# Performance work log

Measured on AMD Instinct MI355X. Metric: run time of the kernel, lower is better.

Reference implementation:

```python
import jax, jax.numpy as jnp
import numpy as np

N_E = 1024      # nconcepts (codebook size)
E_DIM = 64      # cdim (codebook vector dim)
BETA = 0.25
LEGACY = True


def setup_inputs() -> dict:
    key = jax.random.key(0)
    k1, k2, k3 = jax.random.split(key, 3)
    z_ = jax.random.normal(k1, (32, 256, 32, 32), jnp.float32)
    # 1x1 conv dis_modulator: 256 -> 64 channels (stored as [out, in])
    conv_w = jax.random.normal(k2, (64, 256), jnp.float32) / np.sqrt(256.0)
    conv_b = jnp.zeros((64,), jnp.float32)
    # embedding.weight.data.uniform_(-1/n_e, 1/n_e)
    emb = jax.random.uniform(k3, (N_E, E_DIM), jnp.float32, -1.0 / N_E, 1.0 / N_E)
    return {"z_": z_, "conv_w": conv_w, "conv_b": conv_b, "emb": emb}


def _forward(z_, conv_w, conv_b, emb):
    sg = jax.lax.stop_gradient
    # dis_modulator: 1x1 conv == per-pixel linear map  (B,Cin,H,W)->(B,Cout,H,W)
    z = jnp.einsum('bchw,oc->bohw', z_, conv_w) + conv_b[None, :, None, None]
    B = z.shape[0]
    # torch .view(-1, e_dim): row-major flatten of (B,C,H,W) into chunks of e_dim
    zf = z.reshape(-1, E_DIM)  # [B*C*H*W/e_dim, e_dim]

    # contrastive term: mean pairwise cosine similarity of codebook rows
    d1 = emb @ emb.T                                  # [n_e, n_e]
    norms = jnp.linalg.norm(emb, axis=1)              # [n_e]
    cosine = d1 / (norms[:, None] * norms[None, :])
    contrastive = jnp.mean(cosine)

    # squared L2 distances: ||z||^2 + ||e||^2 - 2 z.e
    d = (jnp.sum(zf * zf, axis=1, keepdims=True)
         + jnp.sum(emb * emb, axis=1)[None, :]
         - 2.0 * (zf @ emb.T))                        # [N, n_e]
    idx = jnp.argmin(d, axis=1)                       # [N]
    z_q = emb[idx].reshape(z.shape)

    if LEGACY:
        loss = jnp.mean((sg(z_q) - z) ** 2) + BETA * jnp.mean((z_q - sg(z)) ** 2)
    else:
        loss = BETA * jnp.mean((sg(z_q) - z) ** 2) + jnp.mean((z_q - sg(z)) ** 2)
    # hessian_penalty(G, z_, G_z=z): G is an affine 1x1 conv, so the central
    # second difference G(z+x) - 2G(z) + G(z-x) is identically zero -> penalty = 0.
    loss = loss + contrastive

    # straight-through estimator
    z_q_st = z + sg(z_q - z)

    # replicate source exactly: flat zeros(B*n_e) scattered at codebook indices
    sampled = jnp.zeros((B * N_E,), z.dtype).at[idx].set(1.0).reshape(B, N_E)
    min_idx = idx.reshape(B, -1)
    return z_q_st, loss, sampled, min_idx


def reference(z_, conv_w, conv_b, emb):
    z_q, loss, sampled, min_idx = _forward(z_, conv_w, conv_b, emb)
    return z_q, loss, sampled, min_idx
```

## Files before the change

### kernel.cpp

```cpp
#include <hip/hip_runtime.h>

#define BATCH   32
#define CIN     256
#define COUT    64
#define HW      1024
#define NE      1024
#define ED      64
#define ZTOT    2097152

#define OFF_LOSS 2097152
#define OFF_SAMP 2097153
#define OFF_IDX  2129921

#define CXSTR 68
#define XSTR  68
#define ESTR  132

__global__ __launch_bounds__(256, 4) void k_pre(const float* __restrict__ x,
                                                const float* __restrict__ w,
                                                const float* __restrict__ bias,
                                                float* __restrict__ z,
                                                const float* __restrict__ emb,
                                                float* __restrict__ out_samp,
                                                float* __restrict__ enorm,
                                                float* __restrict__ cpart) {
    __shared__ float SH[64 * CXSTR * 2];
    int bx = blockIdx.x;
    int t  = threadIdx.x;

    if (bx < 512) {
        float* Xs = SH;
        float* Ws = SH + 64 * CXSTR;
        int b  = bx >> 4;
        int p0 = (bx & 15) * 64;
        int pg = t & 15;
        int og = t >> 4;
        float acc[4][4];
        #pragma unroll
        for (int i = 0; i < 4; i++)
            #pragma unroll
            for (int j = 0; j < 4; j++) acc[i][j] = 0.0f;

        for (int c0 = 0; c0 < CIN; c0 += 64) {
            __syncthreads();
            {
                int u = t & 15, cg2 = t >> 4;
                #pragma unroll
                for (int m = 0; m < 4; m++) {
                    int c = cg2 + 16 * m;
                    float4 v = *(const float4*)&x[(size_t)(b * CIN + c0 + c) * HW + p0 + 4 * u];
                    *(float4*)&Xs[c * CXSTR + 4 * u] = v;
                }
                #pragma unroll
                for (int m = 0; m < 4; m++) {
                    int o = cg2 + 16 * m;
                    float4 v = *(const float4*)&w[o * CIN + c0 + 4 * u];
                    Ws[(4 * u + 0) * CXSTR + o] = v.x;
                    Ws[(4 * u + 1) * CXSTR + o] = v.y;
                    Ws[(4 * u + 2) * CXSTR + o] = v.z;
                    Ws[(4 * u + 3) * CXSTR + o] = v.w;
                }
            }
            __syncthreads();
            #pragma unroll 8
            for (int k = 0; k < 64; k++) {
                float4 xv = *(const float4*)&Xs[k * CXSTR + 4 * pg];
                float4 wv = *(const float4*)&Ws[k * CXSTR + 4 * og];
                float xa[4] = {xv.x, xv.y, xv.z, xv.w};
                float wb[4] = {wv.x, wv.y, wv.z, wv.w};
                #pragma unroll
                for (int i = 0; i < 4; i++)
                    #pragma unroll
                    for (int j = 0; j < 4; j++)
                        acc[i][j] = fmaf(xa[i], wb[j], acc[i][j]);
            }
        }
        #pragma unroll
        for (int j = 0; j < 4; j++) {
            int o = 4 * og + j;
            float bv = bias[o];
            float4 out;
            out.x = acc[0][j] + bv;
            out.y = acc[1][j] + bv;
            out.z = acc[2][j] + bv;
            out.w = acc[3][j] + bv;
            *(float4*)&z[(size_t)(b * COUT + o) * HW + p0 + 4 * pg] = out;
        }
        return;
    }
    if (bx < 640) {
        out_samp[(bx - 512) * 256 + t] = 0.0f;
        return;
    }
    if (bx < 656) {
        float* invl = SH;
        float* S    = SH + 64;
        int b2 = bx - 640;
        int i0 = b2 * 64;
        if (t < 64) {
            const float* e = emb + (size_t)(i0 + t) * ED;
            float r8[8];
            #pragma unroll
            for (int s = 0; s < 8; s++) { float xx = e[s]; r8[s] = xx * xx; }
            #pragma unroll
            for (int m = 1; m < 8; m++) {
                #pragma unroll
                for (int s = 0; s < 8; s++) { float xx = e[8 * m + s]; r8[s] += xx * xx; }
            }
            float en = ((r8[0] + r8[1]) + (r8[2] + r8[3])) + ((r8[4] + r8[5]) + (r8[6] + r8[7]));
            invl[t] = 1.0f / sqrtf(en);
        }
        __syncthreads();
        int d = t & 63, q = t >> 6;
        float s = 0.0f;
        #pragma unroll
        for (int m = 0; m < 16; m++) {
            int il = q + 4 * m;
            s = fmaf(emb[(size_t)(i0 + il) * ED + d], invl[il], s);
        }
        S[t] = s;
        __syncthreads();
        if (t < 64)
            cpart[b2 * 64 + t] = (S[t] + S[t + 64]) + (S[t + 128] + S[t + 192]);
        return;
    }
    {
        int j = (bx - 656) * 256 + t;
        const float* e = emb + (size_t)j * ED;
        float r8[8];
        #pragma unroll
        for (int s = 0; s < 8; s++) { float xx = e[s]; r8[s] = xx * xx; }
        #pragma unroll
        for (int m = 1; m < 8; m++) {
            #pragma unroll
            for (int s = 0; s < 8; s++) { float xx = e[8 * m + s]; r8[s] += xx * xx; }
        }
        enorm[j] = ((r8[0] + r8[1]) + (r8[2] + r8[3])) + ((r8[4] + r8[5]) + (r8[6] + r8[7]));
    }
}

__global__ __launch_bounds__(256, 2) void k_dist(const float* __restrict__ z,
                                                 const float* __restrict__ emb,
                                                 const float* __restrict__ enorm,
                                                 float* __restrict__ out_idx,
                                                 float* __restrict__ out_samp,
                                                 float* __restrict__ out_zq,
                                                 float* __restrict__ ssep) {
    __shared__ float zs[64 * XSTR];
    __shared__ float es[64 * ESTR];
    __shared__ float zn_s[64];
    __shared__ float en_s[128];
    __shared__ float redd_s[16 * 64];
    __shared__ int   redj_s[16 * 64];
    __shared__ int   bj_s[64];
    __shared__ float warr[4];
    int t = threadIdx.x;
    int row0 = blockIdx.x * 64;
    int rg = t & 15;
    int cg = t >> 4;

    {
        int k = t & 63, wv = t >> 6;
        #pragma unroll
        for (int m = 0; m < 4; m++) {
            int v = wv + 4 * m;
            float4 val;
            val.x = z[(size_t)(row0 + 4 * v + 0) * ED + k];
            val.y = z[(size_t)(row0 + 4 * v + 1) * ED + k];
            val.z = z[(size_t)(row0 + 4 * v + 2) * ED + k];
            val.w = z[(size_t)(row0 + 4 * v + 3) * ED + k];
            *(float4*)&zs[k * XSTR + 4 * v] = val;
        }
    }
    if (t < 64) {
        const float* zr = z + (size_t)(row0 + t) * ED;
        float r8[8];
        #pragma unroll
        for (int s = 0; s < 8; s++) { float xx = zr[s]; r8[s] = xx * xx; }
        #pragma unroll
        for (int m = 1; m < 8; m++) {
            #pragma unroll
            for (int s = 0; s < 8; s++) { float xx = zr[8 * m + s]; r8[s] += xx * xx; }
        }
        zn_s[t] = ((r8[0] + r8[1]) + (r8[2] + r8[3])) + ((r8[4] + r8[5]) + (r8[6] + r8[7]));
    }

    float bestd[4];
    int   bestj[4];
    #pragma unroll
    for (int i = 0; i < 4; i++) { bestd[i] = __builtin_huge_valf(); bestj[i] = 0; }

    for (int ch = 0; ch < 8; ch++) {
        int c0 = ch * 128;
        __syncthreads();
        {
            int k = t & 63, wv = t >> 6;
            #pragma unroll
            for (int m = 0; m < 8; m++) {
                int v = wv + 4 * m;
                float4 val;
                val.x = emb[(size_t)(c0 + 4 * v + 0) * ED + k];
                val.y = emb[(size_t)(c0 + 4 * v + 1) * ED + k];
                val.z = emb[(size_t)(c0 + 4 * v + 2) * ED + k];
                val.w = emb[(size_t)(c0 + 4 * v + 3) * ED + k];
                *(float4*)&es[k * ESTR + 4 * v] = val;
            }
            if (t < 32) {
                float4 ev4 = *(const float4*)&enorm[c0 + 4 * t];
                *(float4*)&en_s[4 * t] = ev4;
            }
        }
        __syncthreads();

        float acc[4][8];
        #pragma unroll
        for (int i = 0; i < 4; i++)
            #pragma unroll
            for (int j = 0; j < 8; j++) acc[i][j] = 0.0f;

        #pragma unroll 8
        for (int k = 0; k < 64; k++) {
            float4 xv = *(const float4*)&zs[k * XSTR + 4 * rg];
            float4 e0 = *(const float4*)&es[k * ESTR + 8 * cg];
            float4 e1 = *(const float4*)&es[k * ESTR + 8 * cg + 4];
            float xa[4] = {xv.x, xv.y, xv.z, xv.w};
            float eb[8] = {e0.x, e0.y, e0.z, e0.w, e1.x, e1.y, e1.z, e1.w};
            #pragma unroll
            for (int i = 0; i < 4; i++)
                #pragma unroll
                for (int j = 0; j < 8; j++)
                    acc[i][j] = fmaf(xa[i], eb[j], acc[i][j]);
        }

        #pragma unroll
        for (int i = 0; i < 4; i++) {
            float zn = zn_s[4 * rg + i];
            #pragma unroll
            for (int j = 0; j < 8; j++) {
                int cl = 8 * cg + j;
                float A = zn + en_s[cl];
                float D = A - 2.0f * acc[i][j];
                if (D < bestd[i]) { bestd[i] = D; bestj[i] = c0 + cl; }
            }
        }
    }

    #pragma unroll
    for (int i = 0; i < 4; i++) {
        redd_s[cg * 64 + 4 * rg + i] = bestd[i];
        redj_s[cg * 64 + 4 * rg + i] = bestj[i];
    }
    __syncthreads();
    if (t < 64) {
        float bd = __builtin_huge_valf();
        int   bj = 0x7fffffff;
        #pragma unroll
        for (int c = 0; c < 16; c++) {
            float dd = redd_s[c * 64 + t];
            int   jj = redj_s[c * 64 + t];
            if (dd < bd || (dd == bd && jj < bj)) { bd = dd; bj = jj; }
        }
        int rowg = row0 + t;
        bj_s[t]       = bj;
        out_idx[rowg] = (float)bj;
        atomicExch(&out_samp[bj], 1.0f);
    }
    __syncthreads();

    {
        int r  = t & 63;
        int kq = t >> 6;
        int bj = bj_s[r];
        const float* er = emb + (size_t)bj * ED + kq * 16;
        float sq = 0.0f;
        #pragma unroll
        for (int m = 0; m < 4; m++) {
            float4 ev = *(const float4*)&er[4 * m];
            float zv0 = zs[(kq * 16 + 4 * m + 0) * XSTR + r];
            float zv1 = zs[(kq * 16 + 4 * m + 1) * XSTR + r];
            float zv2 = zs[(kq * 16 + 4 * m + 2) * XSTR + r];
            float zv3 = zs[(kq * 16 + 4 * m + 3) * XSTR + r];
            float d0 = ev.x - zv0, d1 = ev.y - zv1, d2 = ev.z - zv2, d3 = ev.w - zv3;
            float4 o4;
            o4.x = zv0 + d0; o4.y = zv1 + d1; o4.z = zv2 + d2; o4.w = zv3 + d3;
            *(float4*)&out_zq[(size_t)(row0 + r) * ED + kq * 16 + 4 * m] = o4;
            sq += d0 * d0; sq += d1 * d1; sq += d2 * d2; sq += d3 * d3;
        }
        #pragma unroll
        for (int off = 32; off > 0; off >>= 1) sq += __shfl_down(sq, off, 64);
        int lane = t & 63, wv = t >> 6;
        if (lane == 0) warr[wv] = sq;
    }
    __syncthreads();
    if (t == 0)
        ssep[blockIdx.x] = (warr[0] + warr[1]) + (warr[2] + warr[3]);
}

__global__ __launch_bounds__(256) void k_final(const float* __restrict__ ssep,
                                               const float* __restrict__ cpart,
                                               float* __restrict__ out_loss) {
    __shared__ double SD[256];
    __shared__ float  CS;
    int t = threadIdx.x;
    SD[t] = (double)ssep[t] + (double)ssep[t + 256];
    __syncthreads();
    #pragma unroll
    for (int off = 128; off > 0; off >>= 1) {
        if (t < off) SD[t] += SD[t + off];
        __syncthreads();
    }
    if (t < 64) {
        float v = 0.0f;
        #pragma unroll
        for (int m = 0; m < 16; m++) v += cpart[m * 64 + t];
        float sq = v * v;
        #pragma unroll
        for (int off = 32; off > 0; off >>= 1) sq += __shfl_down(sq, off, 64);
        if (t == 0) CS = sq / (1024.0f * 1024.0f);
    }
    __syncthreads();
    if (t == 0) {
        float m = (float)(SD[0] / (double)ZTOT);
        float loss = m + 0.25f * m;
        out_loss[0] = loss + CS;
    }
}

extern "C" void kernel_launch(void* const* d_in, const int* in_sizes, int n_in,
                              void* d_out, int out_size, void* d_ws, size_t ws_size,
                              hipStream_t stream) {
    (void)in_sizes; (void)n_in; (void)out_size; (void)ws_size;
    const float* z_     = (const float*)d_in[0];
    const float* conv_w = (const float*)d_in[1];
    const float* conv_b = (const float*)d_in[2];
    const float* emb    = (const float*)d_in[3];

    float* out      = (float*)d_out;
    float* out_zq   = out;
    float* out_loss = out + OFF_LOSS;
    float* out_samp = out + OFF_SAMP;
    float* out_idx  = out + OFF_IDX;

    char*  ws       = (char*)d_ws;
    float* wz       = (float*)ws;
    float* enorm    = (float*)(ws + 8388608);
    float* cpart    = (float*)(ws + 8392704);
    float* ssep     = (float*)(ws + 8396800);

    k_pre  <<<660, 256, 0, stream>>>(z_, conv_w, conv_b, wz, emb, out_samp, enorm, cpart);
    k_dist <<<512, 256, 0, stream>>>(wz, emb, enorm, out_idx, out_samp, out_zq, ssep);
    k_final<<<1,   256, 0, stream>>>(ssep, cpart, out_loss);
}
```

Measured before the change: 158.4 us.

## Register-prefetch next tile of inputs/codebook to overlap global loads with compute

In the 1x1-conv GEMM and the distance/argmin kernel, the next chunk of x/w or codebook rows is loaded into registers right after the shared-memory store barrier, while the current chunk is being computed. The next iteration then only writes registers to LDS. This hides global-memory latency behind FMA work, at the cost of extra registers (32 floats in the distance kernel), which may reduce occupancy.

```diff
diff --git a/kernel.cpp b/kernel.cpp
--- a/kernel.cpp
+++ b/kernel.cpp
@@ -35,33 +35,42 @@
         int p0 = (bx & 15) * 64;
         int pg = t & 15;
         int og = t >> 4;
+        int u  = t & 15, cg2 = t >> 4;
         float acc[4][4];
         #pragma unroll
         for (int i = 0; i < 4; i++)
             #pragma unroll
             for (int j = 0; j < 4; j++) acc[i][j] = 0.0f;
+
+        float4 xst[4], wst[4];
+        #pragma unroll
+        for (int m = 0; m < 4; m++) {
+            int c = cg2 + 16 * m;
+            xst[m] = *(const float4*)&x[(size_t)(b * CIN + c) * HW + p0 + 4 * u];
+            wst[m] = *(const float4*)&w[c * CIN + 4 * u];
+        }
 
         for (int c0 = 0; c0 < CIN; c0 += 64) {
             __syncthreads();
-            {
-                int u = t & 15, cg2 = t >> 4;
+            #pragma unroll
+            for (int m = 0; m < 4; m++) {
+                int c = cg2 + 16 * m;
+                *(float4*)&Xs[c * CXSTR + 4 * u] = xst[m];
+                Ws[(4 * u + 0) * CXSTR + c] = wst[m].x;
+                Ws[(4 * u + 1) * CXSTR + c] = wst[m].y;
+                Ws[(4 * u + 2) * CXSTR + c] = wst[m].z;
+                Ws[(4 * u + 3) * CXSTR + c] = wst[m].w;
+            }
+            __syncthreads();
+            if (c0 < CIN - 64) {
+                int c0n = c0 + 64;
                 #pragma unroll
                 for (int m = 0; m < 4; m++) {
                     int c = cg2 + 16 * m;
-                    float4 v = *(const float4*)&x[(size_t)(b * CIN + c0 + c) * HW + p0 + 4 * u];
-                    *(float4*)&Xs[c * CXSTR + 4 * u] = v;
+                    xst[m] = *(const float4*)&x[(size_t)(b * CIN + c0n + c) * HW + p0 + 4 * u];
+                    wst[m] = *(const float4*)&w[c * CIN + c0n + 4 * u];
                 }
-                #pragma unroll
-                for (int m = 0; m < 4; m++) {
-                    int o = cg2 + 16 * m;
-                    float4 v = *(const float4*)&w[o * CIN + c0 + 4 * u];
-                    Ws[(4 * u + 0) * CXSTR + o] = v.x;
-                    Ws[(4 * u + 1) * CXSTR + o] = v.y;
-                    Ws[(4 * u + 2) * CXSTR + o] = v.z;
-                    Ws[(4 * u + 3) * CXSTR + o] = v.w;
-                }
-            }
-            __syncthreads();
+            }
             #pragma unroll 8
             for (int k = 0; k < 64; k++) {
                 float4 xv = *(const float4*)&Xs[k * CXSTR + 4 * pg];
@@ -158,18 +167,18 @@
     int row0 = blockIdx.x * 64;
     int rg = t & 15;
     int cg = t >> 4;
+    int sk = t & 63, swv = t >> 6;
 
     {
-        int k = t & 63, wv = t >> 6;
         #pragma unroll
         for (int m = 0; m < 4; m++) {
-            int v = wv + 4 * m;
+            int v = swv + 4 * m;
             float4 val;
-            val.x = z[(size_t)(row0 + 4 * v + 0) * ED + k];
-            val.y = z[(size_t)(row0 + 4 * v + 1) * ED + k];
-            val.z = z[(size_t)(row0 + 4 * v + 2) * ED + k];
-            val.w = z[(size_t)(row0 + 4 * v + 3) * ED + k];
-            *(float4*)&zs[k * XSTR + 4 * v] = val;
+            val.x = z[(size_t)(row0 + 4 * v + 0) * ED + sk];
+            val.y = z[(size_t)(row0 + 4 * v + 1) * ED + sk];
+            val.z = z[(size_t)(row0 + 4 * v + 2) * ED + sk];
+            val.w = z[(size_t)(row0 + 4 * v + 3) * ED + sk];
+            *(float4*)&zs[sk * XSTR + 4 * v] = val;
         }
     }
     if (t < 64) {
@@ -184,6 +193,18 @@
         }
         zn_s[t] = ((r8[0] + r8[1]) + (r8[2] + r8[3])) + ((r8[4] + r8[5]) + (r8[6] + r8[7]));
     }
+
+    float st[32];
+    float4 enr;
+    #pragma unroll
+    for (int m = 0; m < 8; m++) {
+        int v = swv + 4 * m;
+        st[4 * m + 0] = emb[(size_t)(4 * v + 0) * ED + sk];
+        st[4 * m + 1] = emb[(size_t)(4 * v + 1) * ED + sk];
+        st[4 * m + 2] = emb[(size_t)(4 * v + 2) * ED + sk];
+        st[4 * m + 3] = emb[(size_t)(4 * v + 3) * ED + sk];
+    }
+    if (t < 32) enr = *(const float4*)&enorm[4 * t];
 
     float bestd[4];
     int   bestj[4];
@@ -194,23 +215,32 @@
         int c0 = ch * 128;
         __syncthreads();
         {
-            int k = t & 63, wv = t >> 6;
             #pragma unroll
             for (int m = 0; m < 8; m++) {
-                int v = wv + 4 * m;
+                int v = swv + 4 * m;
                 float4 val;
-                val.x = emb[(size_t)(c0 + 4 * v + 0) * ED + k];
-                val.y = emb[(size_t)(c0 + 4 * v + 1) * ED + k];
-                val.z = emb[(size_t)(c0 + 4 * v + 2) * ED + k];
-                val.w = emb[(size_t)(c0 + 4 * v + 3) * ED + k];
-                *(float4*)&es[k * ESTR + 4 * v] = val;
-            }
-            if (t < 32) {
-                float4 ev4 = *(const float4*)&enorm[c0 + 4 * t];
-                *(float4*)&en_s[4 * t] = ev4;
-            }
-        }
-        __syncthreads();
+                val.x = st[4 * m + 0];
+                val.y = st[4 * m + 1];
+                val.z = st[4 * m + 2];
+                val.w = st[4 * m + 3];
+                *(float4*)&es[sk * ESTR + 4 * v] = val;
+            }
+            if (t < 32) *(float4*)&en_s[4 * t] = enr;
+        }
+        __syncthreads();
+
+        if (ch < 7) {
+            int c0n = c0 + 128;
+            #pragma unroll
+            for (int m = 0; m < 8; m++) {
+                int v = swv + 4 * m;
+                st[4 * m + 0] = emb[(size_t)(c0n + 4 * v + 0) * ED + sk];
+                st[4 * m + 1] = emb[(size_t)(c0n + 4 * v + 1) * ED + sk];
+                st[4 * m + 2] = emb[(size_t)(c0n + 4 * v + 2) * ED + sk];
+                st[4 * m + 3] = emb[(size_t)(c0n + 4 * v + 3) * ED + sk];
+            }
+            if (t < 32) enr = *(const float4*)&enorm[c0n + 4 * t];
+        }
 
         float acc[4][8];
         #pragma unroll
@@ -288,8 +318,8 @@
         }
         #pragma unroll
         for (int off = 32; off > 0; off >>= 1) sq += __shfl_down(sq, off, 64);
-        int lane = t & 63, wv = t >> 6;
-        if (lane == 0) warr[wv] = sq;
+        int lane = t & 63, wv2 = t >> 6;
+        if (lane == 0) warr[wv2] = sq;
     }
     __syncthreads();
     if (t == 0)
```

New measurement: 164.2 us. 3.7% more time.
